# Performance work log

Hardware: AMD Instinct MI355X
Metric: run time of the kernel (lower is better)

Reference implementation:

```python
import jax, jax.numpy as jnp
import numpy as np

NUM_HEADS = 8
KERNEL = 7  # kernel_size (kh == kw == 7), dilation 1, non-causal


def _na_indices(L, k):
    # NATTEN neighborhood: window start clamped so the kxk window stays in-bounds
    starts = jnp.clip(jnp.arange(L) - k // 2, 0, L - k)  # [L]
    return starts[:, None] + jnp.arange(k)               # [L, k]


def setup_inputs() -> dict:
    key = jax.random.key(0)
    k1, k2, k3 = jax.random.split(key, 3)
    B, H, W, C = 1, 64, 128, 256
    x = jax.random.normal(k1, (B, H, W, C), dtype=jnp.float32)
    # weights stored as [in, out] so y = x @ w + b (equivalent to torch Linear math)
    w_qkv = jax.random.normal(k2, (C, 3 * C), dtype=jnp.float32) * 0.02
    b_qkv = jnp.zeros((3 * C,), dtype=jnp.float32)
    w_proj = jax.random.normal(k3, (C, C), dtype=jnp.float32) * 0.02
    b_proj = jnp.zeros((C,), dtype=jnp.float32)
    return {"x": x, "w_qkv": w_qkv, "b_qkv": b_qkv, "w_proj": w_proj, "b_proj": b_proj}


def reference(x, w_qkv, b_qkv, w_proj, b_proj):
    B, H, W, C = x.shape
    nh = NUM_HEADS
    hd = C // nh
    scale = hd ** -0.5
    kk = KERNEL

    qkv = (x @ w_qkv + b_qkv).reshape(B, H, W, 3, nh, hd)
    q = qkv[:, :, :, 0]  # [B,H,W,nh,hd]
    k = qkv[:, :, :, 1]
    v = qkv[:, :, :, 2]

    ih = _na_indices(H, kk)  # [H,kk]
    iw = _na_indices(W, kk)  # [W,kk]

    # gather K/V neighborhoods: [B,H,kh,W,kw,nh,hd]
    k_win = k[:, ih][:, :, :, iw]
    v_win = v[:, ih][:, :, :, iw]

    # scores: query vs its kh*kw neighbors
    attn = jnp.einsum('bhwnd,bhpwqnd->bhwnpq', q * scale, k_win)  # [B,H,W,nh,kh,kw]
    attn = jax.nn.softmax(attn.reshape(B, H, W, nh, kk * kk), axis=-1)
    attn = attn.reshape(B, H, W, nh, kk, kk)

    out = jnp.einsum('bhwnpq,bhpwqnd->bhwnd', attn, v_win)  # [B,H,W,nh,hd]
    out = out.reshape(B, H, W, C)
    return out @ w_proj + b_proj
```

## Files before the change

### kernel.cpp

```cpp
#include <hip/hip_runtime.h>
#include <cmath>

#define HH 64
#define WW 128
#define CC 256
#define NHEAD 8
#define HDIM 32
#define NPIX (HH*WW)
#define QKV_N (3*CC)

#define KSLOT 248
#define LDK   40
#define VSLOT 264

typedef __attribute__((ext_vector_type(8))) short short8v;
typedef __attribute__((ext_vector_type(4))) short short4v;
typedef __attribute__((ext_vector_type(4))) float f32x4;
typedef unsigned int u32;

__device__ __forceinline__ short f2bf(float f) {
    unsigned int u = __builtin_bit_cast(unsigned int, f);
    u += 0x7fffu + ((u >> 16) & 1u);
    return (short)(u >> 16);
}

__global__ __launch_bounds__(256)
void prep_w(const float* __restrict__ w_qkv, const float* __restrict__ w_proj,
            short* __restrict__ wq_t, short* __restrict__ wp_t)
{
    __shared__ float tile[32][33];
    int idx = blockIdx.x;
    const float* src; short* dst; int N;
    if (idx < 192) { src = w_qkv;  dst = wq_t; N = QKV_N; }
    else { idx -= 192; src = w_proj; dst = wp_t; N = CC; }
    const int nbx = N / 32;
    const int bn = (idx % nbx) * 32;
    const int bk = (idx / nbx) * 32;
    const int tx = threadIdx.x & 31, ty = threadIdx.x >> 5;
#pragma unroll
    for (int i = 0; i < 32; i += 8)
        tile[ty + i][tx] = src[(size_t)(bk + ty + i) * N + bn + tx];
    __syncthreads();
#pragma unroll
    for (int i = 0; i < 32; i += 8)
        dst[(size_t)(bn + ty + i) * CC + bk + tx] = f2bf(tile[tx][ty + i]);
}

__global__ __launch_bounds__(256)
void gemm_qkv(const float* __restrict__ A, const short* __restrict__ Bt,
              const float* __restrict__ bias, short* __restrict__ Cp)
{
    __shared__ short As[64 * 40];
    __shared__ short Bs[2][128 * 32];

    const int tid = threadIdx.x, lane = tid & 63, wave = tid >> 6;
    const int wm0 = (wave >> 1) * 32, wn0 = (wave & 1) * 64;
    const int bm = blockIdx.x * 64, bn = blockIdx.y * 128;
    const int l15 = lane & 15, l4 = lane >> 4;
    const int arow = tid >> 2, akoff = (tid & 3) * 8;

    f32x4 acc[2][4];
#pragma unroll
    for (int i = 0; i < 2; ++i)
#pragma unroll
        for (int j = 0; j < 4; ++j) acc[i][j] = (f32x4){0.f, 0.f, 0.f, 0.f};

    auto stageB = [&](int buf, int t) {
#pragma unroll
        for (int i = 0; i < 2; ++i) {
            const int g = tid + 256 * i;
            const int row = g >> 2, gr = g & 3;
            __builtin_amdgcn_global_load_lds(
                (const __attribute__((address_space(1))) u32*)
                    (Bt + (size_t)(bn + row) * CC + t * 32 + ((gr ^ (row & 3)) * 8)),
                (__attribute__((address_space(3))) u32*)&Bs[buf][g * 8], 16, 0, 0);
        }
    };

    float4 a0, a1;
    {
        const float* p = A + (size_t)(bm + arow) * CC + akoff;
        a0 = *(const float4*)p; a1 = *(const float4*)(p + 4);
    }
    stageB(0, 0);

    for (int t = 0; t < 8; ++t) {
        const int cur = t & 1;
        __syncthreads();
        {
            short8v w;
            w[0] = f2bf(a0.x); w[1] = f2bf(a0.y); w[2] = f2bf(a0.z); w[3] = f2bf(a0.w);
            w[4] = f2bf(a1.x); w[5] = f2bf(a1.y); w[6] = f2bf(a1.z); w[7] = f2bf(a1.w);
            *(short8v*)&As[arow * 40 + akoff] = w;
        }
        __syncthreads();
        if (t + 1 < 8) {
            const float* p = A + (size_t)(bm + arow) * CC + (t + 1) * 32 + akoff;
            a0 = *(const float4*)p; a1 = *(const float4*)(p + 4);
            stageB(cur ^ 1, t + 1);
        }

        short8v af[2], bf[4];
#pragma unroll
        for (int fm = 0; fm < 2; ++fm)
            af[fm] = *(const short8v*)&As[(wm0 + fm * 16 + l15) * 40 + l4 * 8];
#pragma unroll
        for (int fn = 0; fn < 4; ++fn) {
            const int row = wn0 + fn * 16 + l15;
            bf[fn] = *(const short8v*)&Bs[cur][row * 32 + ((l4 ^ (row & 3)) * 8)];
        }
#pragma unroll
        for (int fm = 0; fm < 2; ++fm)
#pragma unroll
            for (int fn = 0; fn < 4; ++fn)
                acc[fm][fn] = __builtin_amdgcn_mfma_f32_16x16x32_bf16(
                    af[fm], bf[fn], acc[fm][fn], 0, 0, 0);
    }

    const int col0 = bn + wn0 + l15;
    const int row0 = bm + wm0 + l4 * 4;
#pragma unroll
    for (int fn = 0; fn < 4; ++fn) {
        const int cc = col0 + fn * 16;
        const float bv = bias[cc];
#pragma unroll
        for (int fm = 0; fm < 2; ++fm)
#pragma unroll
            for (int r = 0; r < 4; ++r) {
                const int rr = row0 + fm * 16 + r;
                Cp[((size_t)(cc >> 5) * NPIX + rr) * HDIM + (cc & 31)] =
                    f2bf(acc[fm][fn][r] + bv);
            }
    }
}

__global__ __launch_bounds__(256)
void gemm_proj(const short* __restrict__ A, const short* __restrict__ Bt,
               const float* __restrict__ bias, float* __restrict__ C)
{
    __shared__ short As[2][64 * 32];
    __shared__ short Bs[2][128 * 32];

    const int tid = threadIdx.x, lane = tid & 63, wave = tid >> 6;
    const int wm0 = (wave >> 1) * 32, wn0 = (wave & 1) * 64;
    const int bm = blockIdx.x * 64, bn = blockIdx.y * 128;
    const int l15 = lane & 15, l4 = lane >> 4;

    f32x4 acc[2][4];
#pragma unroll
    for (int i = 0; i < 2; ++i)
#pragma unroll
        for (int j = 0; j < 4; ++j) acc[i][j] = (f32x4){0.f, 0.f, 0.f, 0.f};

    auto stage = [&](int buf, int t) {
        {
            const int row = tid >> 2, gr = tid & 3;
            __builtin_amdgcn_global_load_lds(
                (const __attribute__((address_space(1))) u32*)
                    (A + (size_t)(bm + row) * CC + t * 32 + ((gr ^ (row & 3)) * 8)),
                (__attribute__((address_space(3))) u32*)&As[buf][tid * 8], 16, 0, 0);
        }
#pragma unroll
        for (int i = 0; i < 2; ++i) {
            const int g = tid + 256 * i;
            const int row = g >> 2, gr = g & 3;
            __builtin_amdgcn_global_load_lds(
                (const __attribute__((address_space(1))) u32*)
                    (Bt + (size_t)(bn + row) * CC + t * 32 + ((gr ^ (row & 3)) * 8)),
                (__attribute__((address_space(3))) u32*)&Bs[buf][g * 8], 16, 0, 0);
        }
    };

    stage(0, 0);

    for (int t = 0; t < 8; ++t) {
        const int cur = t & 1;
        __syncthreads();
        if (t + 1 < 8) stage(cur ^ 1, t + 1);

        short8v af[2], bf[4];
#pragma unroll
        for (int fm = 0; fm < 2; ++fm) {
            const int row = wm0 + fm * 16 + l15;
            af[fm] = *(const short8v*)&As[cur][row * 32 + ((l4 ^ (row & 3)) * 8)];
        }
#pragma unroll
        for (int fn = 0; fn < 4; ++fn) {
            const int row = wn0 + fn * 16 + l15;
            bf[fn] = *(const short8v*)&Bs[cur][row * 32 + ((l4 ^ (row & 3)) * 8)];
        }
#pragma unroll
        for (int fm = 0; fm < 2; ++fm)
#pragma unroll
            for (int fn = 0; fn < 4; ++fn)
                acc[fm][fn] = __builtin_amdgcn_mfma_f32_16x16x32_bf16(
                    af[fm], bf[fn], acc[fm][fn], 0, 0, 0);
    }

    const int col0 = bn + wn0 + l15;
    const int row0 = bm + wm0 + l4 * 4;
#pragma unroll
    for (int fn = 0; fn < 4; ++fn) {
        const float bv = bias[col0 + fn * 16];
#pragma unroll
        for (int fm = 0; fm < 2; ++fm)
#pragma unroll
            for (int r = 0; r < 4; ++r)
                C[(size_t)(row0 + fm * 16 + r) * CC + col0 + fn * 16] =
                    acc[fm][fn][r] + bv;
    }
}

__global__ __launch_bounds__(256)
void na_mfma(const short* __restrict__ qkv, short* __restrict__ attn)
{
    __shared__ short Ksh[KSLOT * LDK];
    __shared__ short Vsh[32 * VSLOT];

    const int x0 = blockIdx.x * 16;
    const int y0 = blockIdx.y * 4;
    const int head = blockIdx.z;
    const int tid = threadIdx.x, lane = tid & 63, w = tid >> 6;
    const int rs  = min(max(y0 - 3, 0), HH - 7);
    const int wsx = x0 - 3;
    const short* Qp = qkv + (size_t)head * NPIX * HDIM;
    const short* Kp = qkv + (size_t)(NHEAD + head) * NPIX * HDIM;
    const short* Vp = qkv + (size_t)(2 * NHEAD + head) * NPIX * HDIM;

    for (int idx = tid; idx < 880; idx += 256) {
        int g = idx & 3, rc = idx >> 2;
        int i = rc / 22, c = rc - i * 22;
        int yy = rs + i, xx = wsx + c;
        if (yy < HH && (unsigned)xx < WW)
            *(short8v*)&Ksh[(i * 24 + c) * LDK + g * 8] =
                *(const short8v*)(Kp + (size_t)(yy * WW + xx) * HDIM + g * 8);
    }
    for (int idx = tid; idx < 264; idx += 256) {
        int g = idx & 3, q2 = idx >> 2;
        int i = q2 / 6, cq = q2 - i * 6;
        int yy = rs + i;
        short8v vv[4];
#pragma unroll
        for (int j = 0; j < 4; ++j) {
            int c = cq * 4 + j, xx = wsx + c;
            if (yy < HH && c < 22 && (unsigned)xx < WW)
                vv[j] = *(const short8v*)(Vp + (size_t)(yy * WW + xx) * HDIM + g * 8);
            else {
                short8v z = {0,0,0,0,0,0,0,0};
                vv[j] = z;
            }
        }
#pragma unroll
        for (int jd = 0; jd < 8; ++jd) {
            short4v s4 = {vv[0][jd], vv[1][jd], vv[2][jd], vv[3][jd]};
            *(short4v*)&Vsh[(g * 8 + jd) * VSLOT + i * 24 + cq * 4] = s4;
        }
    }

    const int l15 = lane & 15, l4 = lane >> 4;
    const int y = y0 + w;
    short8v qf = *(const short8v*)(Qp + (size_t)(y * WW + x0 + l15) * HDIM + l4 * 8);
    __syncthreads();

    const int wbase = (min(max(y - 3, 0), HH - 7) - rs) * 24;

    f32x4 sacc[11];
#pragma unroll
    for (int kc = 0; kc < 11; ++kc) {
        short8v kf = *(const short8v*)&Ksh[(wbase + kc * 16 + l15) * LDK + l4 * 8];
        f32x4 z = {0.f, 0.f, 0.f, 0.f};
        sacc[kc] = __builtin_amdgcn_mfma_f32_16x16x32_bf16(kf, qf, z, 0, 0, 0);
    }

    const int xq = x0 + l15;
    const int cw = min(max(xq - 3, 0), WW - 7) - wsx;
    const float scale = 0.17677669529663687f;
    float lsum = 0.f;
#pragma unroll
    for (int kc = 0; kc < 11; ++kc) {
#pragma unroll
        for (int r = 0; r < 4; ++r) {
            int kl = kc * 16 + l4 * 4 + r;
            int row = kl / 24;
            int c = kl - row * 24;
            bool valid = (row < 7) && (c >= cw) && (c <= cw + 6);
            float e = valid ? __expf(sacc[kc][r] * scale) : 0.f;
            sacc[kc][r] = e;
            lsum += e;
        }
    }
    lsum += __shfl_xor(lsum, 16);
    lsum += __shfl_xor(lsum, 32);
    const float inv = 1.0f / lsum;

    short4v pf[12];
#pragma unroll
    for (int kc = 0; kc < 11; ++kc) {
        short4v pk;
#pragma unroll
        for (int r = 0; r < 4; ++r) pk[r] = f2bf(sacc[kc][r] * inv);
        pf[kc] = pk;
    }
    pf[11] = (short4v){0, 0, 0, 0};

    const int src0 = ((l4 & 1) << 5) + l15;
    const int src1 = src0 + 16;
    const bool hi = (l4 & 2) != 0;
    f32x4 oacc[2];
    oacc[0] = (f32x4){0.f, 0.f, 0.f, 0.f};
    oacc[1] = (f32x4){0.f, 0.f, 0.f, 0.f};
#pragma unroll
    for (int kc2 = 0; kc2 < 6; ++kc2) {
        int lo0 = ((const int*)&pf[2 * kc2])[0];
        int lo1 = ((const int*)&pf[2 * kc2])[1];
        int hi0 = ((const int*)&pf[2 * kc2 + 1])[0];
        int hi1 = ((const int*)&pf[2 * kc2 + 1])[1];
        int a0 = __shfl(lo0, src0), a1 = __shfl(lo1, src0);
        int a2 = __shfl(lo0, src1), a3 = __shfl(lo1, src1);
        int b0 = __shfl(hi0, src0), b1 = __shfl(hi1, src0);
        int b2 = __shfl(hi0, src1), b3 = __shfl(hi1, src1);
        int w0 = hi ? b0 : a0, w1 = hi ? b1 : a1;
        int w2 = hi ? b2 : a2, w3 = hi ? b3 : a3;
        int wv[4] = {w0, w1, w2, w3};
        short8v bfrag = *(const short8v*)wv;
#pragma unroll
        for (int nc = 0; nc < 2; ++nc) {
            short8v vf = *(const short8v*)&Vsh[(nc * 16 + l15) * VSLOT
                                               + wbase + kc2 * 32 + l4 * 8];
            oacc[nc] = __builtin_amdgcn_mfma_f32_16x16x32_bf16(vf, bfrag, oacc[nc], 0, 0, 0);
        }
    }

    short* op = attn + (size_t)(y * WW + x0 + l15) * CC + head * HDIM;
#pragma unroll
    for (int nc = 0; nc < 2; ++nc) {
        short4v o;
#pragma unroll
        for (int r = 0; r < 4; ++r) o[r] = f2bf(oacc[nc][r]);
        *(short4v*)(op + nc * 16 + l4 * 4) = o;
    }
}

extern "C" void kernel_launch(void* const* d_in, const int* in_sizes, int n_in,
                              void* d_out, int out_size, void* d_ws, size_t ws_size,
                              hipStream_t stream)
{
    const float* x      = (const float*)d_in[0];
    const float* w_qkv  = (const float*)d_in[1];
    const float* b_qkv  = (const float*)d_in[2];
    const float* w_proj = (const float*)d_in[3];
    const float* b_proj = (const float*)d_in[4];
    float* out = (float*)d_out;

    char* ws = (char*)d_ws;
    short* qkv_r   = (short*)ws;
    short* attn_bf = (short*)(ws + 12582912);
    short* wq_t    = (short*)(ws + 16777216);
    short* wp_t    = (short*)(ws + 17170432);

    prep_w<<<dim3(256), dim3(256), 0, stream>>>(w_qkv, w_proj, wq_t, wp_t);

    gemm_qkv<<<dim3(NPIX / 64, QKV_N / 128), dim3(256), 0, stream>>>(
        x, wq_t, b_qkv, qkv_r);

    na_mfma<<<dim3(WW / 16, HH / 4, NHEAD), dim3(256), 0, stream>>>(qkv_r, attn_bf);

    gemm_proj<<<dim3(NPIX / 64, CC / 128), dim3(256), 0, stream>>>(
        attn_bf, wp_t, b_proj, out);
}
```

Before: 43.89 us.

## Enlarge NA tiles to 8 rows, double-buffer A in QKV GEMM, drop LDS swizzles

The neighborhood-attention kernel now handles 8 query rows per block with 512 threads, so the K/V halo loaded into shared memory is reused by more queries. The QKV GEMM double-buffers its A tile, which removes one barrier per k-step, and writes its output in a plain pixel-major [NPIX,768] layout instead of a head-major layout. The XOR swizzles on the shared-memory B/A tiles are removed from both GEMMs, which simplifies addressing but may bring back LDS bank conflicts. Q/K/V reads in the attention kernel are now strided by 768 elements per pixel, which may lower gather efficiency.

```diff
diff --git a/kernel.cpp b/kernel.cpp
--- a/kernel.cpp
+++ b/kernel.cpp
@@ -8,10 +8,6 @@
 #define HDIM 32
 #define NPIX (HH*WW)
 #define QKV_N (3*CC)
-
-#define KSLOT 248
-#define LDK   40
-#define VSLOT 264
 
 typedef __attribute__((ext_vector_type(8))) short short8v;
 typedef __attribute__((ext_vector_type(4))) short short4v;
@@ -46,69 +42,70 @@
         dst[(size_t)(bn + ty + i) * CC + bk + tx] = f2bf(tile[tx][ty + i]);
 }
 
+#define LDA 40
+
 __global__ __launch_bounds__(256)
-void gemm_qkv(const float* __restrict__ A, const short* __restrict__ Bt,
-              const float* __restrict__ bias, short* __restrict__ Cp)
-{
-    __shared__ short As[64 * 40];
+void gemm_qkv(const float* __restrict__ x, const short* __restrict__ Bt,
+              const float* __restrict__ bias, short* __restrict__ Cbf)
+{
+    __shared__ short As[2][64 * LDA];
     __shared__ short Bs[2][128 * 32];
 
     const int tid = threadIdx.x, lane = tid & 63, wave = tid >> 6;
+    const int bm = blockIdx.x * 64, bn = blockIdx.y * 128;
     const int wm0 = (wave >> 1) * 32, wn0 = (wave & 1) * 64;
-    const int bm = blockIdx.x * 64, bn = blockIdx.y * 128;
     const int l15 = lane & 15, l4 = lane >> 4;
-    const int arow = tid >> 2, akoff = (tid & 3) * 8;
-
-    f32x4 acc[2][4];
-#pragma unroll
-    for (int i = 0; i < 2; ++i)
-#pragma unroll
-        for (int j = 0; j < 4; ++j) acc[i][j] = (f32x4){0.f, 0.f, 0.f, 0.f};
-
+    const int arow = tid >> 2, ako = (tid & 3) * 8;
+
+    float4 a0, a1;
+    auto loadA = [&](int t) {
+        const float* p = x + (size_t)(bm + arow) * CC + t * 32 + ako;
+        a0 = *(const float4*)p; a1 = *(const float4*)(p + 4);
+    };
+    auto writeA = [&](int buf) {
+        short8v v;
+        v[0] = f2bf(a0.x); v[1] = f2bf(a0.y); v[2] = f2bf(a0.z); v[3] = f2bf(a0.w);
+        v[4] = f2bf(a1.x); v[5] = f2bf(a1.y); v[6] = f2bf(a1.z); v[7] = f2bf(a1.w);
+        *(short8v*)&As[buf][arow * LDA + ako] = v;
+    };
     auto stageB = [&](int buf, int t) {
 #pragma unroll
         for (int i = 0; i < 2; ++i) {
             const int g = tid + 256 * i;
-            const int row = g >> 2, gr = g & 3;
             __builtin_amdgcn_global_load_lds(
                 (const __attribute__((address_space(1))) u32*)
-                    (Bt + (size_t)(bn + row) * CC + t * 32 + ((gr ^ (row & 3)) * 8)),
+                    (Bt + (size_t)(bn + (g >> 2)) * CC + t * 32 + (g & 3) * 8),
                 (__attribute__((address_space(3))) u32*)&Bs[buf][g * 8], 16, 0, 0);
         }
     };
 
-    float4 a0, a1;
-    {
-        const float* p = A + (size_t)(bm + arow) * CC + akoff;
-        a0 = *(const float4*)p; a1 = *(const float4*)(p + 4);
-    }
+    f32x4 acc[2][4];
+#pragma unroll
+    for (int i = 0; i < 2; ++i)
+#pragma unroll
+        for (int j = 0; j < 4; ++j) acc[i][j] = (f32x4){0.f, 0.f, 0.f, 0.f};
+
+    loadA(0);
+    writeA(0);
     stageB(0, 0);
+    loadA(1);
 
     for (int t = 0; t < 8; ++t) {
         const int cur = t & 1;
         __syncthreads();
-        {
-            short8v w;
-            w[0] = f2bf(a0.x); w[1] = f2bf(a0.y); w[2] = f2bf(a0.z); w[3] = f2bf(a0.w);
-            w[4] = f2bf(a1.x); w[5] = f2bf(a1.y); w[6] = f2bf(a1.z); w[7] = f2bf(a1.w);
-            *(short8v*)&As[arow * 40 + akoff] = w;
-        }
-        __syncthreads();
         if (t + 1 < 8) {
-            const float* p = A + (size_t)(bm + arow) * CC + (t + 1) * 32 + akoff;
-            a0 = *(const float4*)p; a1 = *(const float4*)(p + 4);
+            writeA(cur ^ 1);
             stageB(cur ^ 1, t + 1);
+            if (t + 2 < 8) loadA(t + 2);
         }
 
         short8v af[2], bf[4];
 #pragma unroll
         for (int fm = 0; fm < 2; ++fm)
-            af[fm] = *(const short8v*)&As[(wm0 + fm * 16 + l15) * 40 + l4 * 8];
-#pragma unroll
-        for (int fn = 0; fn < 4; ++fn) {
-            const int row = wn0 + fn * 16 + l15;
-            bf[fn] = *(const short8v*)&Bs[cur][row * 32 + ((l4 ^ (row & 3)) * 8)];
-        }
+            af[fm] = *(const short8v*)&As[cur][(wm0 + fm * 16 + l15) * LDA + l4 * 8];
+#pragma unroll
+        for (int fn = 0; fn < 4; ++fn)
+            bf[fn] = *(const short8v*)&Bs[cur][(wn0 + fn * 16 + l15) * 32 + l4 * 8];
 #pragma unroll
         for (int fm = 0; fm < 2; ++fm)
 #pragma unroll
@@ -121,16 +118,13 @@
     const int row0 = bm + wm0 + l4 * 4;
 #pragma unroll
     for (int fn = 0; fn < 4; ++fn) {
-        const int cc = col0 + fn * 16;
-        const float bv = bias[cc];
-#pragma unroll
-        for (int fm = 0; fm < 2; ++fm)
-#pragma unroll
-            for (int r = 0; r < 4; ++r) {
-                const int rr = row0 + fm * 16 + r;
-                Cp[((size_t)(cc >> 5) * NPIX + rr) * HDIM + (cc & 31)] =
+        const float bv = bias[col0 + fn * 16];
+#pragma unroll
+        for (int fm = 0; fm < 2; ++fm)
+#pragma unroll
+            for (int r = 0; r < 4; ++r)
+                Cbf[(size_t)(row0 + fm * 16 + r) * QKV_N + col0 + fn * 16] =
                     f2bf(acc[fm][fn][r] + bv);
-            }
     }
 }
 
@@ -138,12 +132,13 @@
 void gemm_proj(const short* __restrict__ A, const short* __restrict__ Bt,
                const float* __restrict__ bias, float* __restrict__ C)
 {
-    __shared__ short As[2][64 * 32];
-    __shared__ short Bs[2][128 * 32];
+    constexpr int BM = 64, BN = 128, BK = 32;
+    __shared__ short As[2][BM * BK];
+    __shared__ short Bs[2][BN * BK];
 
     const int tid = threadIdx.x, lane = tid & 63, wave = tid >> 6;
     const int wm0 = (wave >> 1) * 32, wn0 = (wave & 1) * 64;
-    const int bm = blockIdx.x * 64, bn = blockIdx.y * 128;
+    const int bm = blockIdx.x * BM, bn = blockIdx.y * BN;
     const int l15 = lane & 15, l4 = lane >> 4;
 
     f32x4 acc[2][4];
@@ -154,19 +149,18 @@
 
     auto stage = [&](int buf, int t) {
         {
-            const int row = tid >> 2, gr = tid & 3;
+            const int g = tid;
             __builtin_amdgcn_global_load_lds(
                 (const __attribute__((address_space(1))) u32*)
-                    (A + (size_t)(bm + row) * CC + t * 32 + ((gr ^ (row & 3)) * 8)),
-                (__attribute__((address_space(3))) u32*)&As[buf][tid * 8], 16, 0, 0);
+                    (A + (size_t)(bm + (g >> 2)) * CC + t * BK + (g & 3) * 8),
+                (__attribute__((address_space(3))) u32*)&As[buf][g * 8], 16, 0, 0);
         }
 #pragma unroll
         for (int i = 0; i < 2; ++i) {
             const int g = tid + 256 * i;
-            const int row = g >> 2, gr = g & 3;
             __builtin_amdgcn_global_load_lds(
                 (const __attribute__((address_space(1))) u32*)
-                    (Bt + (size_t)(bn + row) * CC + t * 32 + ((gr ^ (row & 3)) * 8)),
+                    (Bt + (size_t)(bn + (g >> 2)) * CC + t * BK + (g & 3) * 8),
                 (__attribute__((address_space(3))) u32*)&Bs[buf][g * 8], 16, 0, 0);
         }
     };
@@ -180,15 +174,11 @@
 
         short8v af[2], bf[4];
 #pragma unroll
-        for (int fm = 0; fm < 2; ++fm) {
-            const int row = wm0 + fm * 16 + l15;
-            af[fm] = *(const short8v*)&As[cur][row * 32 + ((l4 ^ (row & 3)) * 8)];
-        }
-#pragma unroll
-        for (int fn = 0; fn < 4; ++fn) {
-            const int row = wn0 + fn * 16 + l15;
-            bf[fn] = *(const short8v*)&Bs[cur][row * 32 + ((l4 ^ (row & 3)) * 8)];
-        }
+        for (int fm = 0; fm < 2; ++fm)
+            af[fm] = *(const short8v*)&As[cur][(wm0 + fm * 16 + l15) * BK + l4 * 8];
+#pragma unroll
+        for (int fn = 0; fn < 4; ++fn)
+            bf[fn] = *(const short8v*)&Bs[cur][(wn0 + fn * 16 + l15) * BK + l4 * 8];
 #pragma unroll
         for (int fm = 0; fm < 2; ++fm)
 #pragma unroll
@@ -211,31 +201,34 @@
     }
 }
 
-__global__ __launch_bounds__(256)
+#define LDK    40
+#define KSLOT2 344
+#define VSLOT2 392
+
+__global__ __launch_bounds__(512)
 void na_mfma(const short* __restrict__ qkv, short* __restrict__ attn)
 {
-    __shared__ short Ksh[KSLOT * LDK];
-    __shared__ short Vsh[32 * VSLOT];
+    __shared__ short Ksh[KSLOT2 * LDK];
+    __shared__ short Vsh[32 * VSLOT2];
 
     const int x0 = blockIdx.x * 16;
-    const int y0 = blockIdx.y * 4;
+    const int y0 = blockIdx.y * 8;
     const int head = blockIdx.z;
     const int tid = threadIdx.x, lane = tid & 63, w = tid >> 6;
     const int rs  = min(max(y0 - 3, 0), HH - 7);
     const int wsx = x0 - 3;
-    const short* Qp = qkv + (size_t)head * NPIX * HDIM;
-    const short* Kp = qkv + (size_t)(NHEAD + head) * NPIX * HDIM;
-    const short* Vp = qkv + (size_t)(2 * NHEAD + head) * NPIX * HDIM;
-
-    for (int idx = tid; idx < 880; idx += 256) {
+
+    for (int idx = tid; idx < 1232; idx += 512) {
         int g = idx & 3, rc = idx >> 2;
         int i = rc / 22, c = rc - i * 22;
         int yy = rs + i, xx = wsx + c;
-        if (yy < HH && (unsigned)xx < WW)
+        if (yy < HH && (unsigned)xx < WW) {
             *(short8v*)&Ksh[(i * 24 + c) * LDK + g * 8] =
-                *(const short8v*)(Kp + (size_t)(yy * WW + xx) * HDIM + g * 8);
-    }
-    for (int idx = tid; idx < 264; idx += 256) {
+                *(const short8v*)(qkv + (size_t)(yy * WW + xx) * QKV_N
+                                  + CC + head * HDIM + g * 8);
+        }
+    }
+    for (int idx = tid; idx < 392; idx += 512) {
         int g = idx & 3, q2 = idx >> 2;
         int i = q2 / 6, cq = q2 - i * 6;
         int yy = rs + i;
@@ -243,8 +236,9 @@
 #pragma unroll
         for (int j = 0; j < 4; ++j) {
             int c = cq * 4 + j, xx = wsx + c;
-            if (yy < HH && c < 22 && (unsigned)xx < WW)
-                vv[j] = *(const short8v*)(Vp + (size_t)(yy * WW + xx) * HDIM + g * 8);
+            if (i < 14 && yy < HH && c < 22 && (unsigned)xx < WW)
+                vv[j] = *(const short8v*)(qkv + (size_t)(yy * WW + xx) * QKV_N
+                                          + 2 * CC + head * HDIM + g * 8);
             else {
                 short8v z = {0,0,0,0,0,0,0,0};
                 vv[j] = z;
@@ -253,13 +247,14 @@
 #pragma unroll
         for (int jd = 0; jd < 8; ++jd) {
             short4v s4 = {vv[0][jd], vv[1][jd], vv[2][jd], vv[3][jd]};
-            *(short4v*)&Vsh[(g * 8 + jd) * VSLOT + i * 24 + cq * 4] = s4;
+            *(short4v*)&Vsh[(g * 8 + jd) * VSLOT2 + q2 * 4] = s4;
         }
     }
 
     const int l15 = lane & 15, l4 = lane >> 4;
     const int y = y0 + w;
-    short8v qf = *(const short8v*)(Qp + (size_t)(y * WW + x0 + l15) * HDIM + l4 * 8);
+    short8v qf = *(const short8v*)(qkv + (size_t)(y * WW + x0 + l15) * QKV_N
+                                   + head * HDIM + l4 * 8);
     __syncthreads();
 
     const int wbase = (min(max(y - 3, 0), HH - 7) - rs) * 24;
@@ -325,7 +320,7 @@
         short8v bfrag = *(const short8v*)wv;
 #pragma unroll
         for (int nc = 0; nc < 2; ++nc) {
-            short8v vf = *(const short8v*)&Vsh[(nc * 16 + l15) * VSLOT
+            short8v vf = *(const short8v*)&Vsh[(nc * 16 + l15) * VSLOT2
                                                + wbase + kc2 * 32 + l4 * 8];
             oacc[nc] = __builtin_amdgcn_mfma_f32_16x16x32_bf16(vf, bfrag, oacc[nc], 0, 0, 0);
         }
@@ -353,7 +348,7 @@
     float* out = (float*)d_out;
 
     char* ws = (char*)d_ws;
-    short* qkv_r   = (short*)ws;
+    short* qkv_bf  = (short*)ws;
     short* attn_bf = (short*)(ws + 12582912);
     short* wq_t    = (short*)(ws + 16777216);
     short* wp_t    = (short*)(ws + 17170432);
@@ -361,9 +356,9 @@
     prep_w<<<dim3(256), dim3(256), 0, stream>>>(w_qkv, w_proj, wq_t, wp_t);
 
     gemm_qkv<<<dim3(NPIX / 64, QKV_N / 128), dim3(256), 0, stream>>>(
-        x, wq_t, b_qkv, qkv_r);
-
-    na_mfma<<<dim3(WW / 16, HH / 4, NHEAD), dim3(256), 0, stream>>>(qkv_r, attn_bf);
+        x, wq_t, b_qkv, qkv_bf);
+
+    na_mfma<<<dim3(WW / 16, HH / 8, NHEAD), dim3(512), 0, stream>>>(qkv_bf, attn_bf);
 
     gemm_proj<<<dim3(NPIX / 64, CC / 128), dim3(256), 0, stream>>>(
         attn_bf, wp_t, b_proj, out);
```

Result: faster. 39.69 us (-9.6%).
